# Optimization experiments

Measured on AMD Instinct MI355X. Metric: run time of the kernel, lower is better.

The kernel has to match this reference:

```python
import jax, jax.numpy as jnp
import numpy as np

H_DIM = 256
NUM_HEADS = 8
HEAD_DIM = H_DIM // NUM_HEADS
BN_EPS = 1e-5
SCALE = float(np.sqrt(HEAD_DIM))


def _lens():
    # 512 graphs, ragged vertex counts cycling 32/64/96/128 -> 40960 total rows
    return np.tile(np.array([32, 64, 96, 128], dtype=np.int64), 128)


def _pad(x, lens):
    # gather ragged rows of x [total, D] into padded [B, Lmax, D]; mask [B, Lmax]
    B = lens.shape[0]
    L = int(lens.max())
    off = np.zeros(B, np.int64)
    off[1:] = np.cumsum(lens)[:-1]
    pos = np.arange(L)
    idx = off[:, None] + np.minimum(pos[None, :], lens[:, None] - 1)
    mask = pos[None, :] < lens[:, None]
    return x[jnp.asarray(idx)], jnp.asarray(mask)


def _flat_idx(lens):
    # (graph_id, position) for every real row, to un-pad back to ragged layout
    b = np.repeat(np.arange(lens.shape[0]), lens)
    i = np.concatenate([np.arange(int(l)) for l in lens])
    return jnp.asarray(b), jnp.asarray(i)


def _forward(src_h, dst_h, src_lens, dst_lens,
             W1, b1, gamma1, beta1, W2, b2, gamma2, beta2):
    src_pad, src_mask = _pad(src_h, src_lens)   # [B, Ls, H]
    dst_pad, _ = _pad(dst_h, dst_lens)          # [B, Ld, H]
    B, Ls, _ = src_pad.shape
    Ld = dst_pad.shape[1]
    # NOTE: original torch code zips self.proj but never applies it, so
    # q = raw dst, k = v = raw src.  The .view(1, head_dim, heads, N) on the
    # channel-major tensor splits feature f as f = d*NUM_HEADS + h.
    q = dst_pad.reshape(B, Ld, HEAD_DIM, NUM_HEADS)
    k = src_pad.reshape(B, Ls, HEAD_DIM, NUM_HEADS)
    v = k
    scores = jnp.einsum('bndh,bmdh->bhnm', q, k) / SCALE
    scores = jnp.where(src_mask[:, None, None, :], scores, jnp.float32(-1e30))
    attn = jax.nn.softmax(scores, axis=-1)
    out = jnp.einsum('bhnm,bmdh->bndh', attn, v).reshape(B, Ld, H_DIM)
    bidx, iidx = _flat_idx(dst_lens)
    h_msg = out[bidx, iidx]                     # [total_dst, H] ragged again
    h = dst_h
    z = jnp.concatenate([h, h_msg], axis=-1)    # [N, 2H]
    y = z @ W1.T + b1
    y = gamma1 * (y - y.mean(0)) * jax.lax.rsqrt(y.var(0) + BN_EPS) + beta1
    y = jax.nn.relu(y)
    y = y @ W2.T + b2
    y = gamma2 * (y - y.mean(0)) * jax.lax.rsqrt(y.var(0) + BN_EPS) + beta2
    return h + y


def setup_inputs() -> dict:
    lens = _lens()
    N = int(lens.sum())
    ks = jax.random.split(jax.random.key(0), 4)
    return {
        'src_h': jax.random.normal(ks[0], (N, H_DIM), jnp.float32),
        'dst_h': jax.random.normal(ks[1], (N, H_DIM), jnp.float32),
        'src_num_verts': jnp.asarray(lens, jnp.int32),
        'dst_num_verts': jnp.asarray(lens, jnp.int32),
        'W1': jax.random.normal(ks[2], (H_DIM, 2 * H_DIM), jnp.float32) / np.float32(np.sqrt(2 * H_DIM)),
        'b1': jnp.zeros((H_DIM,), jnp.float32),
        'gamma1': jnp.ones((H_DIM,), jnp.float32),
        'beta1': jnp.zeros((H_DIM,), jnp.float32),
        'W2': jax.random.normal(ks[3], (H_DIM, H_DIM), jnp.float32) / np.float32(np.sqrt(H_DIM)),
        'b2': jnp.zeros((H_DIM,), jnp.float32),
        'gamma2': jnp.ones((H_DIM,), jnp.float32),
        'beta2': jnp.zeros((H_DIM,), jnp.float32),
    }


def reference(src_h, dst_h, src_num_verts, dst_num_verts,
              W1, b1, gamma1, beta1, W2, b2, gamma2, beta2):
    # segment lengths are static metadata (torch.split takes a Python list)
    src_lens = np.asarray(jax.device_get(src_num_verts), np.int64)
    dst_lens = np.asarray(jax.device_get(dst_num_verts), np.int64)
    return _forward(src_h, dst_h, src_lens, dst_lens,
                    W1, b1, gamma1, beta1, W2, b2, gamma2, beta2)
```

## Files before the change

kernel.cpp:

```cpp
#include <hip/hip_runtime.h>
#include <cstddef>

#define H 256
#define NHEADS 8
#define HD 32

typedef __attribute__((ext_vector_type(8))) short bf16x8;
typedef __attribute__((ext_vector_type(4))) float f32x4;

__device__ __forceinline__ float bf2f(unsigned short s) {
    unsigned u = ((unsigned)s) << 16; return __builtin_bit_cast(float, u);
}
__device__ __forceinline__ float bfe2f(short s) {
    unsigned u = ((unsigned)(unsigned short)s) << 16; return __builtin_bit_cast(float, u);
}
__device__ __forceinline__ unsigned short f2bf(float x) {
    unsigned u = __builtin_bit_cast(unsigned, x);
    u += 0x7fffu + ((u >> 16) & 1u);
    return (unsigned short)(u >> 16);
}
__device__ __forceinline__ void gl_lds16(const void* g, void* l) {
    __builtin_amdgcn_global_load_lds(
        (const __attribute__((address_space(1))) void*)g,
        (__attribute__((address_space(3))) void*)l, 16, 0, 0);
}

__global__ __launch_bounds__(512) void scan_zero_kernel(
    const int* __restrict__ slen, const int* __restrict__ dlen,
    int* __restrict__ soff, int* __restrict__ doff,
    float* __restrict__ stats, int B)
{
    __shared__ int ss[512], dd[512];
    const int t = threadIdx.x;
    const int sv = (t < B) ? slen[t] : 0;
    const int dv = (t < B) ? dlen[t] : 0;
    ss[t] = sv; dd[t] = dv;
    __syncthreads();
    for (int o = 1; o < 512; o <<= 1) {
        int a = (t >= o) ? ss[t - o] : 0;
        int b = (t >= o) ? dd[t - o] : 0;
        __syncthreads();
        ss[t] += a; dd[t] += b;
        __syncthreads();
    }
    if (t < B) { soff[t] = ss[t] - sv; doff[t] = dd[t] - dv; }
    stats[t] = 0.f;
    stats[t + 512] = 0.f;
}

#define PS 2568
__global__ __launch_bounds__(256) void prepass_kernel(
    const float* __restrict__ src, const float* __restrict__ dst,
    unsigned short* __restrict__ KT, unsigned short* __restrict__ VT2,
    unsigned short* __restrict__ QT, int N)
{
    __shared__ unsigned short pl[8 * PS];
    const int t = threadIdx.x;
    const int rb = blockIdx.x * 64;
    const int isrc = (blockIdx.y == 0);
    const float* __restrict__ in = isrc ? src : dst;
    unsigned short* __restrict__ T = isrc ? KT : QT;
    #pragma unroll
    for (int i = 0; i < 16; ++i) {
        const int idx = t + i * 256;
        const int row = idx >> 6, f4 = idx & 63;
        const float4 v = ((const float4*)in)[(size_t)(rb + row) * 64 + f4];
        const int f0 = f4 * 4, h0 = f0 & 7, d = f0 >> 3;
        pl[(h0 + 0) * PS + row * 40 + d] = f2bf(v.x);
        pl[(h0 + 1) * PS + row * 40 + d] = f2bf(v.y);
        pl[(h0 + 2) * PS + row * 40 + d] = f2bf(v.z);
        pl[(h0 + 3) * PS + row * 40 + d] = f2bf(v.w);
    }
    __syncthreads();
    #pragma unroll
    for (int i = 0; i < 8; ++i) {
        const int idx = t + i * 256;
        const int h = idx >> 8, rem = idx & 255, row = rem >> 2, c = rem & 3;
        const bf16x8 val = *(const bf16x8*)&pl[h * PS + row * 40 + c * 8];
        *(bf16x8*)&T[(size_t)(h * N + rb + row) * 32 + c * 8] = val;
    }
    if (isrc) {
        #pragma unroll
        for (int i = 0; i < 8; ++i) {
            const int idx = t + i * 256;
            const int h = idx >> 8, rem = idx & 255, d = rem >> 3, nc = rem & 7;
            bf16x8 v8;
            #pragma unroll
            for (int j = 0; j < 8; ++j)
                v8[j] = (short)pl[h * PS + (nc * 8 + j) * 40 + d];
            *(bf16x8*)&VT2[(size_t)(h * 32 + d) * N + rb + nc * 8] = v8;
        }
    }
}

__global__ __launch_bounds__(256) void cvtW_kernel(
    const float* __restrict__ W1, const float* __restrict__ W2,
    unsigned short* __restrict__ W1p, unsigned short* __restrict__ W2bf)
{
    const int idx = blockIdx.x * 256 + threadIdx.x;
    if (idx < 131072) {
        const int kp = idx & 511, c = idx >> 9;
        const int half = kp >> 8, r = kp & 255, hh = r >> 5, d = r & 31;
        W1p[(size_t)c * 512 + kp] = f2bf(W1[(size_t)c * 512 + half * 256 + d * 8 + hh]);
    } else {
        const int i2 = idx - 131072;
        W2bf[i2] = f2bf(W2[i2]);
    }
}

template<int LS>
__device__ __forceinline__ void attn_body(
    const unsigned short* __restrict__ KT, const unsigned short* __restrict__ QT,
    const unsigned short* __restrict__ VT2, unsigned short* __restrict__ OT,
    unsigned short* __restrict__ Ps, int N, int so, int df, int Ld, int h, int lane)
{
    constexpr int MT = LS / 16, CH = LS / 32;
    const int lr = lane & 15, lq = lane >> 4;
    const float iscale = 0.17677669529663687f;

    bf16x8 kf[MT];
    #pragma unroll
    for (int mt = 0; mt < MT; ++mt)
        kf[mt] = *(const bf16x8*)&KT[(size_t)(h * N + so + mt * 16 + lr) * 32 + lq * 8];
    bf16x8 vf[CH][2];
    #pragma unroll
    for (int c = 0; c < CH; ++c)
        #pragma unroll
        for (int dt = 0; dt < 2; ++dt)
            vf[c][dt] = *(const bf16x8*)&VT2[(size_t)(h * 32 + dt * 16 + lr) * N + so + c * 32 + lq * 8];

    const int NT = Ld >> 4;
    bf16x8 qf = *(const bf16x8*)&QT[(size_t)(h * N + df + lr) * 32 + lq * 8];
    for (int nt = 0; nt < NT; ++nt) {
        bf16x8 qn = qf;
        if (nt + 1 < NT)
            qn = *(const bf16x8*)&QT[(size_t)(h * N + df + (nt + 1) * 16 + lr) * 32 + lq * 8];
        f32x4 s[MT];
        #pragma unroll
        for (int mt = 0; mt < MT; ++mt) {
            f32x4 z = {0.f, 0.f, 0.f, 0.f};
            s[mt] = __builtin_amdgcn_mfma_f32_16x16x32_bf16(kf[mt], qf, z, 0, 0, 0);
        }
        float mx = -INFINITY;
        #pragma unroll
        for (int mt = 0; mt < MT; ++mt)
            mx = fmaxf(mx, fmaxf(fmaxf(s[mt][0], s[mt][1]), fmaxf(s[mt][2], s[mt][3])));
        mx = fmaxf(mx, __shfl_xor(mx, 16));
        mx = fmaxf(mx, __shfl_xor(mx, 32));
        const float mxi = mx * iscale;
        float sum = 0.f;
        #pragma unroll
        for (int mt = 0; mt < MT; ++mt) {
            #pragma unroll
            for (int r = 0; r < 4; ++r) {
                const float e = __expf(s[mt][r] * iscale - mxi);
                s[mt][r] = e; sum += e;
            }
        }
        sum += __shfl_xor(sum, 16);
        sum += __shfl_xor(sum, 32);
        const float rinv = 1.f / sum;
        #pragma unroll
        for (int mt = 0; mt < MT; ++mt) {
            uint2 p;
            p.x = ((unsigned)f2bf(s[mt][0])) | (((unsigned)f2bf(s[mt][1])) << 16);
            p.y = ((unsigned)f2bf(s[mt][2])) | (((unsigned)f2bf(s[mt][3])) << 16);
            *(uint2*)&Ps[lr * 136 + mt * 16 + lq * 4] = p;
        }
        __asm__ volatile("" ::: "memory");
        __builtin_amdgcn_wave_barrier();
        f32x4 o0 = {0.f, 0.f, 0.f, 0.f}, o1 = {0.f, 0.f, 0.f, 0.f};
        #pragma unroll
        for (int c = 0; c < CH; ++c) {
            const bf16x8 pa = *(const bf16x8*)&Ps[lr * 136 + c * 32 + lq * 8];
            o0 = __builtin_amdgcn_mfma_f32_16x16x32_bf16(pa, vf[c][0], o0, 0, 0, 0);
            o1 = __builtin_amdgcn_mfma_f32_16x16x32_bf16(pa, vf[c][1], o1, 0, 0, 0);
        }
        __asm__ volatile("" ::: "memory");
        __builtin_amdgcn_wave_barrier();
        #pragma unroll
        for (int r = 0; r < 4; ++r) {
            const float rv = __shfl(rinv, lq * 4 + r);
            const int row = df + nt * 16 + lq * 4 + r;
            OT[(size_t)(h * N + row) * 32 + lr]      = f2bf(o0[r] * rv);
            OT[(size_t)(h * N + row) * 32 + 16 + lr] = f2bf(o1[r] * rv);
        }
        qf = qn;
    }
}

__global__ __launch_bounds__(256) void attn_mfma(
    const unsigned short* __restrict__ KT, const unsigned short* __restrict__ QT,
    const unsigned short* __restrict__ VT2, unsigned short* __restrict__ OT,
    const int* __restrict__ soff, const int* __restrict__ doff,
    const int* __restrict__ slen, const int* __restrict__ dlen, int N)
{
    __shared__ unsigned short Ps[4][16 * 136];
    const int i = blockIdx.x >> 1, half = blockIdx.x & 1;
    const int grp = i >> 7, j = i & 127;
    const int b = 4 * j + (3 - grp);
    const int w = threadIdx.x >> 6, lane = threadIdx.x & 63;
    const int h = half * 4 + w;
    const int Ls = slen[b], Ld = dlen[b], so = soff[b], df = doff[b];
    switch (Ls) {
        case 32:  attn_body<32> (KT, QT, VT2, OT, Ps[w], N, so, df, Ld, h, lane); break;
        case 64:  attn_body<64> (KT, QT, VT2, OT, Ps[w], N, so, df, Ld, h, lane); break;
        case 96:  attn_body<96> (KT, QT, VT2, OT, Ps[w], N, so, df, Ld, h, lane); break;
        default:  attn_body<128>(KT, QT, VT2, OT, Ps[w], N, so, df, Ld, h, lane); break;
    }
}

__global__ __launch_bounds__(256) void gemm1_mfma(
    const unsigned short* __restrict__ QT, const unsigned short* __restrict__ OT,
    const unsigned short* __restrict__ W, const float* __restrict__ bias,
    unsigned short* __restrict__ out, float* __restrict__ sum, float* __restrict__ sq,
    int N)
{
    __shared__ unsigned short Abuf[2][8 * 512];
    __shared__ unsigned short Bbuf[2][8 * 512];
    const int tid = threadIdx.x;
    const int w = tid >> 6, lane = tid & 63;
    const int rowBase = blockIdx.y * 128, colBase = blockIdx.x * 128;
    const int lr = lane & 15, lq = lane >> 4;
    const int wm = w >> 1, wn = w & 1;

    f32x4 acc[4][4];
    #pragma unroll
    for (int i = 0; i < 4; ++i)
        #pragma unroll
        for (int j = 0; j < 4; ++j) { f32x4 z = {0.f, 0.f, 0.f, 0.f}; acc[i][j] = z; }

    auto stage = [&](int ks, int bi) {
        const unsigned short* __restrict__ Ap = (ks < 8) ? QT : OT;
        const int hh = ks & 7;
        #pragma unroll
        for (int s = 0; s < 2; ++s) {
            const int sub = 2 * w + s;
            gl_lds16(Ap + (size_t)(hh * N + rowBase + sub * 16 + lr) * 32 + lq * 8,
                     &Abuf[bi][sub * 512]);
            gl_lds16(W + (size_t)(colBase + sub * 16 + lr) * 512 + ks * 32 + lq * 8,
                     &Bbuf[bi][sub * 512]);
        }
    };
    auto compute = [&](int bi) {
        bf16x8 af[4], bfr[4];
        #pragma unroll
        for (int i = 0; i < 4; ++i) af[i] = *(const bf16x8*)&Abuf[bi][(wm * 4 + i) * 512 + lane * 8];
        #pragma unroll
        for (int j = 0; j < 4; ++j) bfr[j] = *(const bf16x8*)&Bbuf[bi][(wn * 4 + j) * 512 + lane * 8];
        #pragma unroll
        for (int i = 0; i < 4; ++i)
            #pragma unroll
            for (int j = 0; j < 4; ++j)
                acc[i][j] = __builtin_amdgcn_mfma_f32_16x16x32_bf16(af[i], bfr[j], acc[i][j], 0, 0, 0);
    };

    stage(0, 0);
    stage(1, 1);
    #pragma unroll
    for (int ks = 0; ks < 16; ++ks) {
        if (ks < 15) asm volatile("s_waitcnt vmcnt(4)" ::: "memory");
        else         asm volatile("s_waitcnt vmcnt(0)" ::: "memory");
        __builtin_amdgcn_s_barrier();
        compute(ks & 1);
        asm volatile("s_waitcnt lgkmcnt(0)" ::: "memory");
        __builtin_amdgcn_s_barrier();
        if (ks + 2 < 16) stage(ks + 2, ks & 1);
    }

    const int col0 = colBase + wn * 64;
    #pragma unroll
    for (int j = 0; j < 4; ++j) {
        const int col = col0 + j * 16 + lr;
        const float bv = bias[col];
        float cs = 0.f, cq = 0.f;
        #pragma unroll
        for (int i = 0; i < 4; ++i) {
            const int row0 = rowBase + wm * 64 + i * 16 + lq * 4;
            #pragma unroll
            for (int r = 0; r < 4; ++r) {
                const float v = acc[i][j][r] + bv;
                cs += v; cq += v * v;
                out[(size_t)(row0 + r) * 256 + col] = f2bf(v);
            }
        }
        cs += __shfl_xor(cs, 16); cs += __shfl_xor(cs, 32);
        cq += __shfl_xor(cq, 16); cq += __shfl_xor(cq, 32);
        if (lq == 0) { atomicAdd(&sum[col], cs); atomicAdd(&sq[col], cq); }
    }
}

__global__ __launch_bounds__(256) void gemm2_mfma(
    const unsigned short* __restrict__ A2,
    const unsigned short* __restrict__ W, const float* __restrict__ bias,
    unsigned short* __restrict__ out, float* __restrict__ sum, float* __restrict__ sq)
{
    __shared__ unsigned short Abuf[2][8 * 512];
    __shared__ unsigned short Bbuf[2][8 * 512];
    const int tid = threadIdx.x;
    const int w = tid >> 6, lane = tid & 63;
    const int rowBase = blockIdx.y * 128, colBase = blockIdx.x * 128;
    const int lr = lane & 15, lq = lane >> 4;
    const int wm = w >> 1, wn = w & 1;

    f32x4 acc[4][4];
    #pragma unroll
    for (int i = 0; i < 4; ++i)
        #pragma unroll
        for (int j = 0; j < 4; ++j) { f32x4 z = {0.f, 0.f, 0.f, 0.f}; acc[i][j] = z; }

    auto stage = [&](int ks, int bi) {
        #pragma unroll
        for (int s = 0; s < 2; ++s) {
            const int sub = 2 * w + s;
            gl_lds16(A2 + (size_t)(rowBase + sub * 16 + lr) * 256 + ks * 32 + lq * 8,
                     &Abuf[bi][sub * 512]);
            gl_lds16(W + (size_t)(colBase + sub * 16 + lr) * 256 + ks * 32 + lq * 8,
                     &Bbuf[bi][sub * 512]);
        }
    };
    auto compute = [&](int bi) {
        bf16x8 af[4], bfr[4];
        #pragma unroll
        for (int i = 0; i < 4; ++i) af[i] = *(const bf16x8*)&Abuf[bi][(wm * 4 + i) * 512 + lane * 8];
        #pragma unroll
        for (int j = 0; j < 4; ++j) bfr[j] = *(const bf16x8*)&Bbuf[bi][(wn * 4 + j) * 512 + lane * 8];
        #pragma unroll
        for (int i = 0; i < 4; ++i)
            #pragma unroll
            for (int j = 0; j < 4; ++j)
                acc[i][j] = __builtin_amdgcn_mfma_f32_16x16x32_bf16(af[i], bfr[j], acc[i][j], 0, 0, 0);
    };

    stage(0, 0);
    stage(1, 1);
    #pragma unroll
    for (int ks = 0; ks < 8; ++ks) {
        if (ks < 7) asm volatile("s_waitcnt vmcnt(4)" ::: "memory");
        else        asm volatile("s_waitcnt vmcnt(0)" ::: "memory");
        __builtin_amdgcn_s_barrier();
        compute(ks & 1);
        asm volatile("s_waitcnt lgkmcnt(0)" ::: "memory");
        __builtin_amdgcn_s_barrier();
        if (ks + 2 < 8) stage(ks + 2, ks & 1);
    }

    const int col0 = colBase + wn * 64;
    #pragma unroll
    for (int j = 0; j < 4; ++j) {
        const int col = col0 + j * 16 + lr;
        const float bv = bias[col];
        float cs = 0.f, cq = 0.f;
        #pragma unroll
        for (int i = 0; i < 4; ++i) {
            const int row0 = rowBase + wm * 64 + i * 16 + lq * 4;
            #pragma unroll
            for (int r = 0; r < 4; ++r) {
                const float v = acc[i][j][r] + bv;
                cs += v; cq += v * v;
                out[(size_t)(row0 + r) * 256 + col] = f2bf(v);
            }
        }
        cs += __shfl_xor(cs, 16); cs += __shfl_xor(cs, 32);
        cq += __shfl_xor(cq, 16); cq += __shfl_xor(cq, 32);
        if (lq == 0) { atomicAdd(&sum[col], cs); atomicAdd(&sq[col], cq); }
    }
}

__global__ __launch_bounds__(256) void bnrelu_kernel(
    const unsigned short* __restrict__ y1,
    const float* __restrict__ sum, const float* __restrict__ sq,
    const float* __restrict__ gamma, const float* __restrict__ beta,
    unsigned short* __restrict__ out, int n8, float invN)
{
    const int i = blockIdx.x * 256 + threadIdx.x;
    if (i >= n8) return;
    const int j0 = (i & 31) * 8;
    const bf16x8 yv = ((const bf16x8*)y1)[i];
    short res[8];
    #pragma unroll
    for (int j = 0; j < 8; ++j) {
        const float mean = sum[j0 + j] * invN;
        const float var  = sq[j0 + j] * invN - mean * mean;
        const float rstd = rsqrtf(var + 1e-5f);
        const float sc = gamma[j0 + j] * rstd;
        const float sh = beta[j0 + j] - mean * sc;
        res[j] = (short)f2bf(fmaxf(bfe2f(yv[j]) * sc + sh, 0.f));
    }
    bf16x8 o;
    #pragma unroll
    for (int j = 0; j < 8; ++j) o[j] = res[j];
    ((bf16x8*)out)[i] = o;
}

__global__ __launch_bounds__(256) void epilogue_kernel(
    const float* __restrict__ dst, const unsigned short* __restrict__ y2,
    const float* __restrict__ sum, const float* __restrict__ sq,
    const float* __restrict__ gamma, const float* __restrict__ beta,
    float* __restrict__ out, int n8, float invN)
{
    const int i = blockIdx.x * 256 + threadIdx.x;
    if (i >= n8) return;
    const int j0 = (i & 31) * 8;
    const bf16x8 yv = ((const bf16x8*)y2)[i];
    const float4 d0 = ((const float4*)dst)[2 * i];
    const float4 d1 = ((const float4*)dst)[2 * i + 1];
    float o[8];
    const float dv[8] = {d0.x, d0.y, d0.z, d0.w, d1.x, d1.y, d1.z, d1.w};
    #pragma unroll
    for (int j = 0; j < 8; ++j) {
        const float mean = sum[j0 + j] * invN;
        const float var  = sq[j0 + j] * invN - mean * mean;
        const float rstd = rsqrtf(var + 1e-5f);
        const float sc = gamma[j0 + j] * rstd;
        const float sh = beta[j0 + j] - mean * sc;
        o[j] = dv[j] + bfe2f(yv[j]) * sc + sh;
    }
    float4 o0, o1;
    o0.x = o[0]; o0.y = o[1]; o0.z = o[2]; o0.w = o[3];
    o1.x = o[4]; o1.y = o[5]; o1.z = o[6]; o1.w = o[7];
    ((float4*)out)[2 * i]     = o0;
    ((float4*)out)[2 * i + 1] = o1;
}

extern "C" void kernel_launch(void* const* d_in, const int* in_sizes, int n_in,
                              void* d_out, int out_size, void* d_ws, size_t ws_size,
                              hipStream_t stream)
{
    const float* src_h  = (const float*)d_in[0];
    const float* dst_h  = (const float*)d_in[1];
    const int*   slen   = (const int*)d_in[2];
    const int*   dlen   = (const int*)d_in[3];
    const float* W1     = (const float*)d_in[4];
    const float* b1     = (const float*)d_in[5];
    const float* gamma1 = (const float*)d_in[6];
    const float* beta1  = (const float*)d_in[7];
    const float* W2     = (const float*)d_in[8];
    const float* b2     = (const float*)d_in[9];
    const float* gamma2 = (const float*)d_in[10];
    const float* beta2  = (const float*)d_in[11];
    float* out = (float*)d_out;

    const int N = in_sizes[1] / H;
    const int B = in_sizes[2];

    char* base = (char*)d_ws;
    int*   soff   = (int*)(base + 0);
    int*   doff   = (int*)(base + 2048);
    float* stats  = (float*)(base + 4096);
    unsigned short* W1p  = (unsigned short*)(base + 16384);
    unsigned short* W2bf = (unsigned short*)(base + 16384 + 262144);
    const size_t S = (size_t)N * H * sizeof(unsigned short);
    char* big = base + (1 << 20);
    unsigned short* KT  = (unsigned short*)(big);
    unsigned short* VT2 = (unsigned short*)(big + S);
    unsigned short* QT  = (unsigned short*)(big + 2 * S);
    unsigned short* OT  = (unsigned short*)(big + 3 * S);
    unsigned short* y1bf = KT;
    unsigned short* a2   = VT2;
    unsigned short* y2bf = QT;

    const float invN = 1.0f / (float)N;

    scan_zero_kernel<<<1, 512, 0, stream>>>(slen, dlen, soff, doff, stats, B);

    prepass_kernel<<<dim3(N / 64, 2), 256, 0, stream>>>(src_h, dst_h, KT, VT2, QT, N);
    cvtW_kernel<<<768, 256, 0, stream>>>(W1, W2, W1p, W2bf);

    attn_mfma<<<B * 2, 256, 0, stream>>>(KT, QT, VT2, OT, soff, doff, slen, dlen, N);

    dim3 ggrid(H / 128, N / 128);
    gemm1_mfma<<<ggrid, 256, 0, stream>>>(QT, OT, W1p, b1, y1bf, stats + 0, stats + 256, N);

    const int n8 = N * H / 8;
    bnrelu_kernel<<<(n8 + 255) / 256, 256, 0, stream>>>(
        y1bf, stats + 0, stats + 256, gamma1, beta1, a2, n8, invN);

    gemm2_mfma<<<ggrid, 256, 0, stream>>>(a2, W2bf, b2, y2bf, stats + 512, stats + 768);

    epilogue_kernel<<<(n8 + 255) / 256, 256, 0, stream>>>(
        dst_h, y2bf, stats + 512, stats + 768, gamma2, beta2, out, n8, invN);
}
```

Baseline: 276.5 us.

## Fuse preprocessing kernels and fold BN1+ReLU into GEMM2 A-operand load

Merges the scan, input transpose/convert and weight conversion kernels into one launch, with a warp-shuffle scan replacing the shared-memory scan. The BN1+ReLU pass is removed: GEMM2 now loads raw y1 into registers, applies scale/shift/ReLU and writes the result to LDS, which avoids a full read/write round trip of the activation. The GEMM1 pipeline is rewritten to a simpler two-buffer loop built on __syncthreads, and the LDS row pitch in the prepass changes to reduce bank conflicts. Costs are extra VALU work and register pressure in GEMM2, plus possibly less overlap from the simpler barriers.

```diff
diff --git a/kernel.cpp b/kernel.cpp
--- a/kernel.cpp
+++ b/kernel.cpp
@@ -25,86 +25,94 @@
         (__attribute__((address_space(3))) void*)l, 16, 0, 0);
 }
 
-__global__ __launch_bounds__(512) void scan_zero_kernel(
+#define PS 2696
+__global__ __launch_bounds__(256) void pre_kernel(
+    const float* __restrict__ src, const float* __restrict__ dst,
+    const float* __restrict__ W1, const float* __restrict__ W2,
     const int* __restrict__ slen, const int* __restrict__ dlen,
+    unsigned short* __restrict__ KT, unsigned short* __restrict__ VT2,
+    unsigned short* __restrict__ QT,
+    unsigned short* __restrict__ W1p, unsigned short* __restrict__ W2bf,
     int* __restrict__ soff, int* __restrict__ doff,
-    float* __restrict__ stats, int B)
-{
-    __shared__ int ss[512], dd[512];
-    const int t = threadIdx.x;
-    const int sv = (t < B) ? slen[t] : 0;
-    const int dv = (t < B) ? dlen[t] : 0;
-    ss[t] = sv; dd[t] = dv;
-    __syncthreads();
-    for (int o = 1; o < 512; o <<= 1) {
-        int a = (t >= o) ? ss[t - o] : 0;
-        int b = (t >= o) ? dd[t - o] : 0;
-        __syncthreads();
-        ss[t] += a; dd[t] += b;
-        __syncthreads();
-    }
-    if (t < B) { soff[t] = ss[t] - sv; doff[t] = dd[t] - dv; }
-    stats[t] = 0.f;
-    stats[t + 512] = 0.f;
-}
-
-#define PS 2568
-__global__ __launch_bounds__(256) void prepass_kernel(
-    const float* __restrict__ src, const float* __restrict__ dst,
-    unsigned short* __restrict__ KT, unsigned short* __restrict__ VT2,
-    unsigned short* __restrict__ QT, int N)
+    float* __restrict__ stats, int N, int B)
 {
     __shared__ unsigned short pl[8 * PS];
     const int t = threadIdx.x;
-    const int rb = blockIdx.x * 64;
-    const int isrc = (blockIdx.y == 0);
-    const float* __restrict__ in = isrc ? src : dst;
-    unsigned short* __restrict__ T = isrc ? KT : QT;
-    #pragma unroll
-    for (int i = 0; i < 16; ++i) {
-        const int idx = t + i * 256;
-        const int row = idx >> 6, f4 = idx & 63;
-        const float4 v = ((const float4*)in)[(size_t)(rb + row) * 64 + f4];
-        const int f0 = f4 * 4, h0 = f0 & 7, d = f0 >> 3;
-        pl[(h0 + 0) * PS + row * 40 + d] = f2bf(v.x);
-        pl[(h0 + 1) * PS + row * 40 + d] = f2bf(v.y);
-        pl[(h0 + 2) * PS + row * 40 + d] = f2bf(v.z);
-        pl[(h0 + 3) * PS + row * 40 + d] = f2bf(v.w);
-    }
-    __syncthreads();
-    #pragma unroll
-    for (int i = 0; i < 8; ++i) {
-        const int idx = t + i * 256;
-        const int h = idx >> 8, rem = idx & 255, row = rem >> 2, c = rem & 3;
-        const bf16x8 val = *(const bf16x8*)&pl[h * PS + row * 40 + c * 8];
-        *(bf16x8*)&T[(size_t)(h * N + rb + row) * 32 + c * 8] = val;
-    }
-    if (isrc) {
+    const int bid = blockIdx.x;
+    const int prepB = N >> 5;
+
+    if (bid < prepB) {
+        const int rb = (bid >> 1) * 64;
+        const int isrc = (bid & 1) == 0;
+        const float* __restrict__ in = isrc ? src : dst;
+        unsigned short* __restrict__ T = isrc ? KT : QT;
+        #pragma unroll
+        for (int i = 0; i < 16; ++i) {
+            const int idx = t + i * 256;
+            const int row = idx >> 6, f4 = idx & 63;
+            const float4 v = ((const float4*)in)[(size_t)(rb + row) * 64 + f4];
+            const int f0 = f4 * 4, h0 = f0 & 7, d = f0 >> 3;
+            pl[(h0 + 0) * PS + row * 42 + d] = f2bf(v.x);
+            pl[(h0 + 1) * PS + row * 42 + d] = f2bf(v.y);
+            pl[(h0 + 2) * PS + row * 42 + d] = f2bf(v.z);
+            pl[(h0 + 3) * PS + row * 42 + d] = f2bf(v.w);
+        }
+        __syncthreads();
         #pragma unroll
         for (int i = 0; i < 8; ++i) {
             const int idx = t + i * 256;
-            const int h = idx >> 8, rem = idx & 255, d = rem >> 3, nc = rem & 7;
-            bf16x8 v8;
-            #pragma unroll
-            for (int j = 0; j < 8; ++j)
-                v8[j] = (short)pl[h * PS + (nc * 8 + j) * 40 + d];
-            *(bf16x8*)&VT2[(size_t)(h * 32 + d) * N + rb + nc * 8] = v8;
-        }
-    }
-}
-
-__global__ __launch_bounds__(256) void cvtW_kernel(
-    const float* __restrict__ W1, const float* __restrict__ W2,
-    unsigned short* __restrict__ W1p, unsigned short* __restrict__ W2bf)
-{
-    const int idx = blockIdx.x * 256 + threadIdx.x;
-    if (idx < 131072) {
-        const int kp = idx & 511, c = idx >> 9;
-        const int half = kp >> 8, r = kp & 255, hh = r >> 5, d = r & 31;
-        W1p[(size_t)c * 512 + kp] = f2bf(W1[(size_t)c * 512 + half * 256 + d * 8 + hh]);
+            const int h = idx >> 8, rem = idx & 255, row = rem >> 2, c = rem & 3;
+            const bf16x8 val = *(const bf16x8*)&pl[h * PS + row * 42 + c * 8];
+            *(bf16x8*)&T[(size_t)(h * N + rb + row) * 32 + c * 8] = val;
+        }
+        if (isrc) {
+            #pragma unroll
+            for (int i = 0; i < 8; ++i) {
+                const int idx = t + i * 256;
+                const int h = idx >> 8, rem = idx & 255, d = rem >> 3, nc = rem & 7;
+                bf16x8 v8;
+                #pragma unroll
+                for (int j = 0; j < 8; ++j)
+                    v8[j] = (short)pl[h * PS + (nc * 8 + j) * 42 + d];
+                *(bf16x8*)&VT2[(size_t)(h * 32 + d) * N + rb + nc * 8] = v8;
+            }
+        }
+    } else if (bid < prepB + 768) {
+        const int idx = (bid - prepB) * 256 + t;
+        if (idx < 131072) {
+            const int kp = idx & 511, c = idx >> 9;
+            const int half = kp >> 8, r = kp & 255, hh = r >> 5, d = r & 31;
+            W1p[(size_t)c * 512 + kp] = f2bf(W1[(size_t)c * 512 + half * 256 + d * 8 + hh]);
+        } else {
+            const int i2 = idx - 131072;
+            W2bf[i2] = f2bf(W2[i2]);
+        }
     } else {
-        const int i2 = idx - 131072;
-        W2bf[i2] = f2bf(W2[i2]);
+        stats[t] = 0.f; stats[t + 256] = 0.f; stats[t + 512] = 0.f; stats[t + 768] = 0.f;
+        if (t < 64) {
+            int sv[8], dv[8];
+            int sl = 0, dl = 0;
+            #pragma unroll
+            for (int j = 0; j < 8; ++j) {
+                const int g = t * 8 + j;
+                sv[j] = sl; dv[j] = dl;
+                sl += (g < B) ? slen[g] : 0;
+                dl += (g < B) ? dlen[g] : 0;
+            }
+            int sx = sl, dx = dl;
+            #pragma unroll
+            for (int o = 1; o < 64; o <<= 1) {
+                const int sy = __shfl_up(sx, o);
+                const int dy = __shfl_up(dx, o);
+                if (t >= o) { sx += sy; dx += dy; }
+            }
+            const int sbase = sx - sl, dbase = dx - dl;
+            #pragma unroll
+            for (int j = 0; j < 8; ++j) {
+                const int g = t * 8 + j;
+                if (g < B) { soff[g] = sbase + sv[j]; doff[g] = dbase + dv[j]; }
+            }
+        }
     }
 }
 
@@ -256,16 +264,14 @@
     };
 
     stage(0, 0);
-    stage(1, 1);
-    #pragma unroll
-    for (int ks = 0; ks < 16; ++ks) {
-        if (ks < 15) asm volatile("s_waitcnt vmcnt(4)" ::: "memory");
-        else         asm volatile("s_waitcnt vmcnt(0)" ::: "memory");
-        __builtin_amdgcn_s_barrier();
-        compute(ks & 1);
-        asm volatile("s_waitcnt lgkmcnt(0)" ::: "memory");
-        __builtin_amdgcn_s_barrier();
-        if (ks + 2 < 16) stage(ks + 2, ks & 1);
+    __syncthreads();
+    for (int ks = 0; ks < 16; ks += 2) {
+        stage(ks + 1, 1);
+        compute(0);
+        __syncthreads();
+        if (ks + 2 < 16) stage(ks + 2, 0);
+        compute(1);
+        __syncthreads();
     }
 
     const int col0 = colBase + wn * 64;
@@ -290,31 +296,62 @@
     }
 }
 
-__global__ __launch_bounds__(256) void gemm2_mfma(
-    const unsigned short* __restrict__ A2,
+__global__ __launch_bounds__(256) void gemm2_fused(
+    const unsigned short* __restrict__ y1,
     const unsigned short* __restrict__ W, const float* __restrict__ bias,
-    unsigned short* __restrict__ out, float* __restrict__ sum, float* __restrict__ sq)
+    const float* __restrict__ sum1, const float* __restrict__ sq1,
+    const float* __restrict__ gamma1, const float* __restrict__ beta1,
+    unsigned short* __restrict__ out, float* __restrict__ sum, float* __restrict__ sq,
+    float invN)
 {
     __shared__ unsigned short Abuf[2][8 * 512];
     __shared__ unsigned short Bbuf[2][8 * 512];
+    __shared__ float scs[256], shs[256];
     const int tid = threadIdx.x;
     const int w = tid >> 6, lane = tid & 63;
     const int rowBase = blockIdx.y * 128, colBase = blockIdx.x * 128;
     const int lr = lane & 15, lq = lane >> 4;
     const int wm = w >> 1, wn = w & 1;
 
+    {
+        const float mean = sum1[tid] * invN;
+        const float var  = sq1[tid] * invN - mean * mean;
+        const float rstd = rsqrtf(var + 1e-5f);
+        const float sc = gamma1[tid] * rstd;
+        scs[tid] = sc;
+        shs[tid] = beta1[tid] - mean * sc;
+    }
+
     f32x4 acc[4][4];
     #pragma unroll
     for (int i = 0; i < 4; ++i)
         #pragma unroll
         for (int j = 0; j < 4; ++j) { f32x4 z = {0.f, 0.f, 0.f, 0.f}; acc[i][j] = z; }
 
-    auto stage = [&](int ks, int bi) {
+    bf16x8 rawA[2];
+    auto loadA = [&](int ks) {
         #pragma unroll
         for (int s = 0; s < 2; ++s) {
             const int sub = 2 * w + s;
-            gl_lds16(A2 + (size_t)(rowBase + sub * 16 + lr) * 256 + ks * 32 + lq * 8,
-                     &Abuf[bi][sub * 512]);
+            rawA[s] = *(const bf16x8*)&y1[(size_t)(rowBase + sub * 16 + lr) * 256 + ks * 32 + lq * 8];
+        }
+    };
+    auto writeA = [&](int ks, int bi) {
+        const int k0 = ks * 32 + lq * 8;
+        #pragma unroll
+        for (int s = 0; s < 2; ++s) {
+            const int sub = 2 * w + s;
+            bf16x8 o;
+            #pragma unroll
+            for (int j = 0; j < 8; ++j)
+                o[j] = (short)f2bf(fmaxf(bfe2f(rawA[s][j]) * scs[k0 + j] + shs[k0 + j], 0.f));
+            *(bf16x8*)&Abuf[bi][sub * 512 + lane * 8] = o;
+        }
+    };
+    auto stageB = [&](int ks, int bi) {
+        #pragma unroll
+        for (int s = 0; s < 2; ++s) {
+            const int sub = 2 * w + s;
             gl_lds16(W + (size_t)(colBase + sub * 16 + lr) * 256 + ks * 32 + lq * 8,
                      &Bbuf[bi][sub * 512]);
         }
@@ -332,17 +369,15 @@
                 acc[i][j] = __builtin_amdgcn_mfma_f32_16x16x32_bf16(af[i], bfr[j], acc[i][j], 0, 0, 0);
     };
 
-    stage(0, 0);
-    stage(1, 1);
-    #pragma unroll
+    __syncthreads();
+    loadA(0); stageB(0, 0); writeA(0, 0);
+    __syncthreads();
     for (int ks = 0; ks < 8; ++ks) {
-        if (ks < 7) asm volatile("s_waitcnt vmcnt(4)" ::: "memory");
-        else        asm volatile("s_waitcnt vmcnt(0)" ::: "memory");
-        __builtin_amdgcn_s_barrier();
-        compute(ks & 1);
-        asm volatile("s_waitcnt lgkmcnt(0)" ::: "memory");
-        __builtin_amdgcn_s_barrier();
-        if (ks + 2 < 8) stage(ks + 2, ks & 1);
+        const int cur = ks & 1;
+        if (ks + 1 < 8) { loadA(ks + 1); stageB(ks + 1, cur ^ 1); }
+        compute(cur);
+        if (ks + 1 < 8) writeA(ks + 1, cur ^ 1);
+        __syncthreads();
     }
 
     const int col0 = colBase + wn * 64;
@@ -365,32 +400,6 @@
         cq += __shfl_xor(cq, 16); cq += __shfl_xor(cq, 32);
         if (lq == 0) { atomicAdd(&sum[col], cs); atomicAdd(&sq[col], cq); }
     }
-}
-
-__global__ __launch_bounds__(256) void bnrelu_kernel(
-    const unsigned short* __restrict__ y1,
-    const float* __restrict__ sum, const float* __restrict__ sq,
-    const float* __restrict__ gamma, const float* __restrict__ beta,
-    unsigned short* __restrict__ out, int n8, float invN)
-{
-    const int i = blockIdx.x * 256 + threadIdx.x;
-    if (i >= n8) return;
-    const int j0 = (i & 31) * 8;
-    const bf16x8 yv = ((const bf16x8*)y1)[i];
-    short res[8];
-    #pragma unroll
-    for (int j = 0; j < 8; ++j) {
-        const float mean = sum[j0 + j] * invN;
-        const float var  = sq[j0 + j] * invN - mean * mean;
-        const float rstd = rsqrtf(var + 1e-5f);
-        const float sc = gamma[j0 + j] * rstd;
-        const float sh = beta[j0 + j] - mean * sc;
-        res[j] = (short)f2bf(fmaxf(bfe2f(yv[j]) * sc + sh, 0.f));
-    }
-    bf16x8 o;
-    #pragma unroll
-    for (int j = 0; j < 8; ++j) o[j] = res[j];
-    ((bf16x8*)out)[i] = o;
 }
 
 __global__ __launch_bounds__(256) void epilogue_kernel(
@@ -457,27 +466,25 @@
     unsigned short* QT  = (unsigned short*)(big + 2 * S);
     unsigned short* OT  = (unsigned short*)(big + 3 * S);
     unsigned short* y1bf = KT;
-    unsigned short* a2   = VT2;
     unsigned short* y2bf = QT;
 
     const float invN = 1.0f / (float)N;
 
-    scan_zero_kernel<<<1, 512, 0, stream>>>(slen, dlen, soff, doff, stats, B);
-
-    prepass_kernel<<<dim3(N / 64, 2), 256, 0, stream>>>(src_h, dst_h, KT, VT2, QT, N);
-    cvtW_kernel<<<768, 256, 0, stream>>>(W1, W2, W1p, W2bf);
+    const int prepB = N >> 5;
+    pre_kernel<<<prepB + 768 + 1, 256, 0, stream>>>(
+        src_h, dst_h, W1, W2, slen, dlen,
+        KT, VT2, QT, W1p, W2bf, soff, doff, stats, N, B);
 
     attn_mfma<<<B * 2, 256, 0, stream>>>(KT, QT, VT2, OT, soff, doff, slen, dlen, N);
 
     dim3 ggrid(H / 128, N / 128);
     gemm1_mfma<<<ggrid, 256, 0, stream>>>(QT, OT, W1p, b1, y1bf, stats + 0, stats + 256, N);
 
+    gemm2_fused<<<ggrid, 256, 0, stream>>>(
+        y1bf, W2bf, b2, stats + 0, stats + 256, gamma1, beta1,
+        y2bf, stats + 512, stats + 768, invN);
+
     const int n8 = N * H / 8;
-    bnrelu_kernel<<<(n8 + 255) / 256, 256, 0, stream>>>(
-        y1bf, stats + 0, stats + 256, gamma1, beta1, a2, n8, invN);
-
-    gemm2_mfma<<<ggrid, 256, 0, stream>>>(a2, W2bf, b2, y2bf, stats + 512, stats + 768);
-
     epilogue_kernel<<<(n8 + 255) / 256, 256, 0, stream>>>(
         dst_h, y2bf, stats + 512, stats + 768, gamma2, beta2, out, n8, invN);
 }
```

Result: faster. 249.6 us (-9.7%).
